# Optimization experiments

Measured on AMD Instinct MI355X. Metric: run time of the kernel, lower is better.

Reference implementation:

```python
import jax, jax.numpy as jnp
import numpy as np
from jax import lax


def _conv(x, w, padding):
    # NCHW conv, stride 1
    return lax.conv_general_dilated(
        x, w, window_strides=(1, 1), padding=padding,
        dimension_numbers=("NCHW", "OIHW", "NCHW"))


def setup_inputs() -> dict:
    key = jax.random.key(0)
    ks = jax.random.split(key, 6)
    B, C_IN, H, W = 128, 2, 64, 64
    L_H, L_Q = 150, 10
    return {
        "X":   jax.random.normal(ks[0], (B, C_IN, H, W), jnp.float32),
        "h_w": jax.random.normal(ks[1], (L_H, C_IN, 3, 3), jnp.float32) * 0.1,
        "h_b": jax.random.normal(ks[2], (L_H,), jnp.float32) * 0.1,
        "r_w": jax.random.normal(ks[3], (1, L_H, 1, 1), jnp.float32) * 0.1,
        "q_w": jax.random.normal(ks[4], (L_Q, 1, 3, 3), jnp.float32) * 0.1,
        "w":   jax.random.normal(ks[5], (L_Q, 1, 3, 3), jnp.float32) * 0.1,
        "k":   40,
    }


def reference(X, h_w, h_b, r_w, q_w, w, k):
    # h = Conv3x3(X) + bias ; r = Conv1x1(h) ; q = Conv3x3(r)
    h = _conv(X, h_w, "SAME") + h_b[None, :, None, None]   # [B, l_h, H, W]
    r = _conv(h, r_w, "VALID")                             # [B, 1, H, W]
    q = _conv(r, q_w, "SAME")                              # [B, l_q, H, W]
    v = jnp.max(q, axis=1, keepdims=True)                  # [B, 1, H, W]

    qw_cat = jnp.concatenate([q_w, w], axis=1)             # [l_q, 2, 3, 3]

    def body(i, v):
        rv = jnp.concatenate([r, v], axis=1)               # [B, 2, H, W]
        q = _conv(rv, qw_cat, "SAME")                      # [B, l_q, H, W]
        return jnp.max(q, axis=1, keepdims=True)

    v = lax.fori_loop(0, k - 1, body, v)
    return v
```

## Files before the change

kernel.cpp:

```cpp
#include <hip/hip_runtime.h>

typedef float f2 __attribute__((ext_vector_type(2)));

#define HW 64
#define XR (66*64)
#define LH 150
#define LQ 10

__device__ __forceinline__ float dpp_wshr1(float x) {
    return __builtin_bit_cast(float, __builtin_amdgcn_update_dpp(
        0, __builtin_bit_cast(int, x), 0x138, 0xF, 0xF, true));
}
__device__ __forceinline__ float dpp_wshl1(float x) {
    return __builtin_bit_cast(float, __builtin_amdgcn_update_dpp(
        0, __builtin_bit_cast(int, x), 0x130, 0xF, 0xF, true));
}
__device__ __forceinline__ f2 dpp2_shr(f2 v) { return (f2){dpp_wshr1(v.x), dpp_wshr1(v.y)}; }
__device__ __forceinline__ f2 dpp2_shl(f2 v) { return (f2){dpp_wshl1(v.x), dpp_wshl1(v.y)}; }

__device__ __forceinline__ f2 pk_fma_b0(f2 a, f2 wpair, f2 c) {
    f2 d;
    asm("v_pk_fma_f32 %0, %1, %2, %3 op_sel_hi:[1,0,1]"
        : "=v"(d) : "v"(a), "s"(wpair), "v"(c));
    return d;
}
__device__ __forceinline__ f2 pk_fma_b1(f2 a, f2 wpair, f2 c) {
    f2 d;
    asm("v_pk_fma_f32 %0, %1, %2, %3 op_sel:[0,1,0]"
        : "=v"(d) : "v"(a), "s"(wpair), "v"(c));
    return d;
}

__global__ __launch_bounds__(1024)
void vin_main(const float* __restrict__ X,
              const float* __restrict__ h_w,
              const float* __restrict__ h_b,
              const float* __restrict__ r_w,
              const float* __restrict__ q_w,
              const float* __restrict__ wgt,
              const int* __restrict__ kptr,
              float* __restrict__ out) {
    __shared__ float smem[3*XR + 32];
    float* sR  = smem + 2*XR;
    float* sWE = smem + 3*XR;
    float* sHB = smem;
    float* sHT = smem + 2176;

    const int b = blockIdx.x, tid = threadIdx.x;
    const int w = tid >> 6, l = tid & 63;

    for (int i = tid; i < 3*XR + 32; i += 1024) smem[i] = 0.f;
    __syncthreads();

    #pragma unroll
    for (int i = 0; i < 2; ++i) {
        int j = w + 16*i;
        if (j < 19) {
            float s = 0.f;
            #pragma unroll
            for (int u = 0; u < 3; ++u) {
                int t = l + 64*u;
                if (t < LH) {
                    float src = (j < 18) ? h_w[t*18 + j] : h_b[t];
                    s = fmaf(r_w[t], src, s);
                }
            }
            #pragma unroll
            for (int off = 32; off >= 1; off >>= 1)
                s += __shfl_xor(s, off);
            if (l == 0) sWE[j] = s;
        }
    }

    const float* Xb = X + (size_t)b * 2 * HW * HW;
    for (int i = tid; i < 2*64*16; i += 1024) {
        int ch = i >> 10, j = i & 1023, row = j >> 4, c = j & 15;
        float4 v = *(const float4*)(Xb + ((size_t)ch*HW + row)*HW + c*4);
        *(float4*)(smem + ch*XR + (row+1)*64 + c*4) = v;
    }
    __syncthreads();

    float wE[19];
    #pragma unroll
    for (int i = 0; i < 19; ++i) wE[i] = sWE[i];
    float rloc[4];
    {
        float xc[2][6], xl[2][6], xr[2][6];
        #pragma unroll
        for (int ch = 0; ch < 2; ++ch)
            #pragma unroll
            for (int k = 0; k < 6; ++k) {
                xc[ch][k] = smem[ch*XR + (4*w + k)*64 + l];
                xl[ch][k] = dpp_wshr1(xc[ch][k]);
                xr[ch][k] = dpp_wshl1(xc[ch][k]);
            }
        #pragma unroll
        for (int i = 0; i < 4; ++i) {
            float acc = wE[18];
            #pragma unroll
            for (int ch = 0; ch < 2; ++ch)
                #pragma unroll
                for (int dy = 0; dy < 3; ++dy) {
                    acc = fmaf(xl[ch][i+dy], wE[ch*9 + dy*3 + 0], acc);
                    acc = fmaf(xc[ch][i+dy], wE[ch*9 + dy*3 + 1], acc);
                    acc = fmaf(xr[ch][i+dy], wE[ch*9 + dy*3 + 2], acc);
                }
            rloc[i] = acc;
        }
    }
    #pragma unroll
    for (int i = 0; i < 4; ++i) sR[(4*w + i + 1)*64 + l] = rloc[i];
    __syncthreads();

    f2 qr[LQ][2];
    f2 vc[2];
    {
        float rc[6], rl[6], rr2[6];
        #pragma unroll
        for (int k = 0; k < 6; ++k) {
            rc[k]  = sR[(4*w + k)*64 + l];
            rl[k]  = dpp_wshr1(rc[k]);
            rr2[k] = dpp_wshl1(rc[k]);
        }
        float vcur[4];
        #pragma unroll
        for (int a = 0; a < LQ; ++a) {
            float qa[9];
            #pragma unroll
            for (int i = 0; i < 9; ++i) qa[i] = q_w[a*9 + i];
            float acc[4];
            #pragma unroll
            for (int i = 0; i < 4; ++i) {
                float s = 0.f;
                #pragma unroll
                for (int dy = 0; dy < 3; ++dy) {
                    s = fmaf(rl[i+dy],  qa[dy*3 + 0], s);
                    s = fmaf(rc[i+dy],  qa[dy*3 + 1], s);
                    s = fmaf(rr2[i+dy], qa[dy*3 + 2], s);
                }
                acc[i] = s;
                vcur[i] = a ? fmaxf(vcur[i], s) : s;
            }
            qr[a][0] = (f2){acc[0], acc[1]};
            qr[a][1] = (f2){acc[2], acc[3]};
        }
        vc[0] = (f2){vcur[0], vcur[1]};
        vc[1] = (f2){vcur[2], vcur[3]};
    }
    if (tid < 256) {
        int p = tid >> 7, half = (tid >> 6) & 1, ll = tid & 63;
        if (half == 0) sHB[p*1088 + 0*64  + ll] = 0.f;
        else           sHT[p*1088 + 16*64 + ll] = 0.f;
    }

    f2 wv2[LQ][5];
    #pragma unroll
    for (int a = 0; a < LQ; ++a) {
        #pragma unroll
        for (int p = 0; p < 4; ++p)
            wv2[a][p] = (f2){wgt[a*9 + 2*p], wgt[a*9 + 2*p + 1]};
        wv2[a][4] = (f2){wgt[a*9 + 8], 0.f};
    }

    const int km1 = kptr[0] - 1;
    const int wrB = (w+1)*64 + l;
    const int wrT = w*64 + l;
    for (int t = 0; t < km1; ++t) {
        const int p = (t & 1) * 1088;
        sHB[p + wrB] = vc[1].y;
        sHT[p + wrT] = vc[0].x;
        __syncthreads();
        float ht = sHB[p + wrT];
        float hb = sHT[p + wrB];

        f2 P[3];
        P[0] = (f2){ht,       vc[0].x};
        P[1] = (f2){vc[0].y,  vc[1].x};
        P[2] = (f2){vc[1].y,  hb};
        f2 PL[3], PR[3], OL[2], OR[2];
        #pragma unroll
        for (int j = 0; j < 3; ++j) { PL[j] = dpp2_shr(P[j]); PR[j] = dpp2_shl(P[j]); }
        #pragma unroll
        for (int j = 0; j < 2; ++j) { OL[j] = dpp2_shr(vc[j]); OR[j] = dpp2_shl(vc[j]); }

        f2 vn[2];
        #pragma unroll
        for (int a = 0; a < LQ; ++a) {
            #pragma unroll
            for (int j = 0; j < 2; ++j) {
                f2 acc = qr[a][j];
                acc = pk_fma_b0(PL[j],   wv2[a][0], acc);
                acc = pk_fma_b1(P[j],    wv2[a][0], acc);
                acc = pk_fma_b0(PR[j],   wv2[a][1], acc);
                acc = pk_fma_b1(OL[j],   wv2[a][1], acc);
                acc = pk_fma_b0(vc[j],   wv2[a][2], acc);
                acc = pk_fma_b1(OR[j],   wv2[a][2], acc);
                acc = pk_fma_b0(PL[j+1], wv2[a][3], acc);
                acc = pk_fma_b1(P[j+1],  wv2[a][3], acc);
                acc = pk_fma_b0(PR[j+1], wv2[a][4], acc);
                vn[j] = (a == 0) ? acc : __builtin_elementwise_max(vn[j], acc);
            }
        }
        vc[0] = vn[0]; vc[1] = vn[1];
    }

    float* ob = out + (size_t)b*HW*HW + (size_t)(4*w)*HW + l;
    ob[0*HW] = vc[0].x;
    ob[1*HW] = vc[0].y;
    ob[2*HW] = vc[1].x;
    ob[3*HW] = vc[1].y;
}

extern "C" void kernel_launch(void* const* d_in, const int* in_sizes, int n_in,
                              void* d_out, int out_size, void* d_ws, size_t ws_size,
                              hipStream_t stream) {
    const float* X   = (const float*)d_in[0];
    const float* h_w = (const float*)d_in[1];
    const float* h_b = (const float*)d_in[2];
    const float* r_w = (const float*)d_in[3];
    const float* q_w = (const float*)d_in[4];
    const float* w   = (const float*)d_in[5];
    const int*   k   = (const int*)d_in[6];
    float* out = (float*)d_out;

    vin_main<<<128, 1024, 0, stream>>>(X, h_w, h_b, r_w, q_w, w, k, out);
}
```

Baseline: 146.0 us.

## Compute halo-independent conv taps before barrier to overlap sync latency

Splits each iteration's 3x3 conv so that all taps not needing neighbour-wave halo rows are accumulated before the __syncthreads, and only the halo-dependent taps run after the barrier. The goal is to hide the barrier and LDS halo exchange latency behind useful FMA work. In exchange it keeps 20 extra packed accumulators live across the barrier, which raises register pressure in a 1024-thread block and may cause spills.

Result: slower. 151.5 us (+3.7%).

```diff
diff --git a/kernel.cpp b/kernel.cpp
--- a/kernel.cpp
+++ b/kernel.cpp
@@ -169,39 +169,54 @@
         const int p = (t & 1) * 1088;
         sHB[p + wrB] = vc[1].y;
         sHT[p + wrT] = vc[0].x;
+
+        f2 P1  = (f2){vc[0].y, vc[1].x};
+        f2 PL1 = dpp2_shr(P1),    PR1 = dpp2_shl(P1);
+        f2 OL0 = dpp2_shr(vc[0]), OR0 = dpp2_shl(vc[0]);
+        f2 OL1 = dpp2_shr(vc[1]), OR1 = dpp2_shl(vc[1]);
+        f2 vn[LQ][2];
+        #pragma unroll
+        for (int a = 0; a < LQ; ++a) {
+            f2 a0 = qr[a][0];
+            a0 = pk_fma_b1(OL0,   wv2[a][1], a0);
+            a0 = pk_fma_b0(vc[0], wv2[a][2], a0);
+            a0 = pk_fma_b1(OR0,   wv2[a][2], a0);
+            a0 = pk_fma_b0(PL1,   wv2[a][3], a0);
+            a0 = pk_fma_b1(P1,    wv2[a][3], a0);
+            a0 = pk_fma_b0(PR1,   wv2[a][4], a0);
+            f2 a1 = qr[a][1];
+            a1 = pk_fma_b0(PL1,   wv2[a][0], a1);
+            a1 = pk_fma_b1(P1,    wv2[a][0], a1);
+            a1 = pk_fma_b0(PR1,   wv2[a][1], a1);
+            a1 = pk_fma_b1(OL1,   wv2[a][1], a1);
+            a1 = pk_fma_b0(vc[1], wv2[a][2], a1);
+            a1 = pk_fma_b1(OR1,   wv2[a][2], a1);
+            vn[a][0] = a0; vn[a][1] = a1;
+        }
+
         __syncthreads();
+
         float ht = sHB[p + wrT];
         float hb = sHT[p + wrB];
-
-        f2 P[3];
-        P[0] = (f2){ht,       vc[0].x};
-        P[1] = (f2){vc[0].y,  vc[1].x};
-        P[2] = (f2){vc[1].y,  hb};
-        f2 PL[3], PR[3], OL[2], OR[2];
-        #pragma unroll
-        for (int j = 0; j < 3; ++j) { PL[j] = dpp2_shr(P[j]); PR[j] = dpp2_shl(P[j]); }
-        #pragma unroll
-        for (int j = 0; j < 2; ++j) { OL[j] = dpp2_shr(vc[j]); OR[j] = dpp2_shl(vc[j]); }
-
-        f2 vn[2];
+        f2 P0  = (f2){ht,       vc[0].x};
+        f2 P2  = (f2){vc[1].y,  hb};
+        f2 PL0 = dpp2_shr(P0), PR0 = dpp2_shl(P0);
+        f2 PL2 = dpp2_shr(P2), PR2 = dpp2_shl(P2);
+        f2 m0, m1;
         #pragma unroll
         for (int a = 0; a < LQ; ++a) {
-            #pragma unroll
-            for (int j = 0; j < 2; ++j) {
-                f2 acc = qr[a][j];
-                acc = pk_fma_b0(PL[j],   wv2[a][0], acc);
-                acc = pk_fma_b1(P[j],    wv2[a][0], acc);
-                acc = pk_fma_b0(PR[j],   wv2[a][1], acc);
-                acc = pk_fma_b1(OL[j],   wv2[a][1], acc);
-                acc = pk_fma_b0(vc[j],   wv2[a][2], acc);
-                acc = pk_fma_b1(OR[j],   wv2[a][2], acc);
-                acc = pk_fma_b0(PL[j+1], wv2[a][3], acc);
-                acc = pk_fma_b1(P[j+1],  wv2[a][3], acc);
-                acc = pk_fma_b0(PR[j+1], wv2[a][4], acc);
-                vn[j] = (a == 0) ? acc : __builtin_elementwise_max(vn[j], acc);
-            }
-        }
-        vc[0] = vn[0]; vc[1] = vn[1];
+            f2 a0 = vn[a][0];
+            a0 = pk_fma_b0(PL0, wv2[a][0], a0);
+            a0 = pk_fma_b1(P0,  wv2[a][0], a0);
+            a0 = pk_fma_b0(PR0, wv2[a][1], a0);
+            f2 a1 = vn[a][1];
+            a1 = pk_fma_b0(PL2, wv2[a][3], a1);
+            a1 = pk_fma_b1(P2,  wv2[a][3], a1);
+            a1 = pk_fma_b0(PR2, wv2[a][4], a1);
+            m0 = (a == 0) ? a0 : __builtin_elementwise_max(m0, a0);
+            m1 = (a == 0) ? a1 : __builtin_elementwise_max(m1, a1);
+        }
+        vc[0] = m0; vc[1] = m1;
     }
 
     float* ob = out + (size_t)b*HW*HW + (size_t)(4*w)*HW + l;
```
